# Kernel tuning notes

Measured on AMD Instinct MI355X. Metric: run time of the kernel, lower is better.

## Reference

```python
import jax, jax.numpy as jnp
import numpy as np

K = 3      # kernel size
PAD = 1    # padding
EPS = 1e-5 # BatchNorm eps


def conv3x3(x, w, b):
    out = jax.lax.conv_general_dilated(
        x, w, window_strides=(1, 1), padding=((PAD, PAD), (PAD, PAD)),
        dimension_numbers=('NCHW', 'OIHW', 'NCHW'))
    return out + b[None, :, None, None]


def bilinear_gather(x, py, px):
    # x: [B,C,H,W]; py,px: [B,K2,H,W] fractional sample coords (zero pad OOB)
    B, C, H, W = x.shape
    y0 = jnp.floor(py)
    x0 = jnp.floor(px)
    wy1 = py - y0
    wx1 = px - x0
    xf = x.reshape(B, C, H * W)

    def corner(yc, xc, wgt):
        valid = (yc >= 0) & (yc <= H - 1) & (xc >= 0) & (xc <= W - 1)
        yi = jnp.clip(yc, 0, H - 1).astype(jnp.int32)
        xi = jnp.clip(xc, 0, W - 1).astype(jnp.int32)
        idx = yi * W + xi                      # [B,K2,H,W]
        g = jax.vmap(lambda img, ix: jnp.take(img, ix, axis=1))(xf, idx.reshape(B, -1))
        g = g.reshape(B, C, idx.shape[1], H, W)  # [B,C,K2,H,W]
        return g * (wgt * valid)[:, None]

    return (corner(y0,     x0,     (1 - wy1) * (1 - wx1))
            + corner(y0,     x0 + 1, (1 - wy1) * wx1)
            + corner(y0 + 1, x0,     wy1 * (1 - wx1))
            + corner(y0 + 1, x0 + 1, wy1 * wx1))


def deform_conv_bn_relu(x, offset_w, offset_b, mod_w, mod_b, weight, bias, gamma, beta):
    B, Ci, H, W = x.shape
    Co = weight.shape[0]
    K2 = K * K
    # offset / modulator branches (dense 3x3 convs)
    off = conv3x3(x, offset_w, offset_b)                  # [B,2*K2,H,W]
    mask = 2.0 * jax.nn.sigmoid(conv3x3(x, mod_w, mod_b))  # [B,K2,H,W]
    off = off.reshape(B, K2, 2, H, W)
    dy, dx = off[:, :, 0], off[:, :, 1]
    # base sampling grid per kernel tap
    ii, jj = jnp.meshgrid(jnp.arange(K), jnp.arange(K), indexing='ij')
    ky = ii.reshape(-1).astype(x.dtype)                    # [K2]
    kx = jj.reshape(-1).astype(x.dtype)
    hh = jnp.arange(H, dtype=x.dtype)
    ww = jnp.arange(W, dtype=x.dtype)
    py = hh[None, None, :, None] - PAD + ky[None, :, None, None] + dy  # [B,K2,H,W]
    px = ww[None, None, None, :] - PAD + kx[None, :, None, None] + dx
    sampled = bilinear_gather(x, py, px)                   # [B,Ci,K2,H,W]
    sampled = sampled * mask[:, None]                      # modulated (DCNv2)
    out = jnp.einsum('bckhw,ock->bohw', sampled, weight.reshape(Co, Ci, K2))
    out = out + bias[None, :, None, None]
    # BatchNorm (batch statistics) + ReLU
    mu = out.mean(axis=(0, 2, 3), keepdims=True)
    var = out.var(axis=(0, 2, 3), keepdims=True)
    y = (out - mu) * jax.lax.rsqrt(var + EPS) * gamma[None, :, None, None] + beta[None, :, None, None]
    return jax.nn.relu(y)


def setup_inputs() -> dict:
    key = jax.random.key(0)
    ks = jax.random.split(key, 4)
    B, Ci, Co, H, W = 8, 256, 256, 64, 64
    x = jax.random.normal(ks[0], (B, Ci, H, W), jnp.float32)
    offset_w = jax.random.normal(ks[1], (2 * K * K, Ci, K, K), jnp.float32) * 0.01
    offset_b = jnp.zeros((2 * K * K,), jnp.float32)
    mod_w = jax.random.normal(ks[2], (K * K, Ci, K, K), jnp.float32) * 0.01
    mod_b = jnp.zeros((K * K,), jnp.float32)
    weight = jax.random.normal(ks[3], (Co, Ci, K, K), jnp.float32) * (1.0 / np.sqrt(Ci * K * K))
    bias = jnp.zeros((Co,), jnp.float32)
    gamma = jnp.ones((Co,), jnp.float32)
    beta = jnp.zeros((Co,), jnp.float32)
    return {"x": x, "offset_w": offset_w, "offset_b": offset_b,
            "mod_w": mod_w, "mod_b": mod_b, "weight": weight, "bias": bias,
            "gamma": gamma, "beta": beta}


def reference(x, offset_w, offset_b, mod_w, mod_b, weight, bias, gamma, beta):
    return deform_conv_bn_relu(x, offset_w, offset_b, mod_w, mod_b, weight, bias, gamma, beta)
```

## Files before the change

kernel.cpp:

```cpp
#include <hip/hip_runtime.h>
#include <math.h>

#define CI 256
#define CO 256
#define HWN 4096

typedef short bf16x8 __attribute__((ext_vector_type(8)));
typedef float f32x4 __attribute__((ext_vector_type(4)));

__device__ inline unsigned pk2(float a, float b) {
  unsigned ua = __float_as_uint(a), ub = __float_as_uint(b);
  ua += 0x7fff + ((ua >> 16) & 1);
  ub += 0x7fff + ((ub >> 16) & 1);
  return (ua >> 16) | (ub & 0xffff0000u);
}

#define PIPE_BARRIER()                                    \
  do {                                                    \
    __builtin_amdgcn_sched_barrier(0);                    \
    asm volatile("s_waitcnt lgkmcnt(0)" ::: "memory");    \
    __builtin_amdgcn_s_barrier();                         \
    __builtin_amdgcn_sched_barrier(0);                    \
  } while (0)

__global__ __launch_bounds__(256) void k_xprep(const float4* __restrict__ xf,
                                               uint4* __restrict__ xh) {
  int i = blockIdx.x * 256 + threadIdx.x;
  float4 a = xf[2 * i], b = xf[2 * i + 1];
  xh[i] = make_uint4(pk2(a.x, a.y), pk2(a.z, a.w), pk2(b.x, b.y),
                     pk2(b.z, b.w));
}

__global__ __launch_bounds__(256) void k_wprep(const float* __restrict__ wgt,
                                               unsigned short* __restrict__ wT) {
  const int o = blockIdx.x, c = threadIdx.x;
  const float* wp = wgt + o * 2304 + c * 9;
  float v[9];
#pragma unroll
  for (int t = 0; t < 9; ++t) v[t] = wp[t];
#pragma unroll
  for (int t = 0; t < 9; ++t) {
    unsigned u = __float_as_uint(v[t]);
    u += 0x7fff + ((u >> 16) & 1);
    wT[(t << 16) + (o << 8) + c] = (unsigned short)(u >> 16);
  }
}

__global__ __launch_bounds__(256) void k_woprep(
    const float* __restrict__ ow, const float* __restrict__ mw,
    unsigned short* __restrict__ wTo) {
  const int o = blockIdx.x, c = threadIdx.x;
  float v[9];
  if (o < 18) {
    const float* wp = ow + o * 2304 + c * 9;
#pragma unroll
    for (int t = 0; t < 9; ++t) v[t] = wp[t];
  } else if (o < 27) {
    const float* wp = mw + (o - 18) * 2304 + c * 9;
#pragma unroll
    for (int t = 0; t < 9; ++t) v[t] = wp[t];
  } else {
#pragma unroll
    for (int t = 0; t < 9; ++t) v[t] = 0.f;
  }
#pragma unroll
  for (int t = 0; t < 9; ++t) {
    unsigned u = __float_as_uint(v[t]);
    u += 0x7fff + ((u >> 16) & 1);
    wTo[(t << 13) + (o << 8) + c] = (unsigned short)(u >> 16);
  }
}

__global__ __launch_bounds__(256, 4) void k_offmod_m(
    const unsigned short* __restrict__ xh, const unsigned short* __restrict__ wTo,
    const float* __restrict__ ob, const float* __restrict__ mb,
    float* __restrict__ dyb, float* __restrict__ dxb,
    float* __restrict__ mskb) {
  __shared__ __align__(16) unsigned s_cwo[576];
  __shared__ unsigned short s_cio[576];
  __shared__ __align__(16) char sA[8192];
  __shared__ __align__(16) char sB[4096];

  const int tid = threadIdx.x;
  const int bid = blockIdx.x;
  const int b = bid >> 6, h = bid & 63;
  const int lane = tid & 63;
  const int wv = tid >> 6;
  const int px = lane;

  for (int i = tid; i < 576; i += 256) {
    int k = i >> 6, pxi = i & 63;
    int ky = k / 3, kx = k - 3 * ky;
    int y0 = h - 1 + ky;
    int x0 = pxi - 1 + kx;
    bool vy = ((unsigned)y0 < 64u);
    bool vx = ((unsigned)x0 < 64u);
    float w00 = (vy && vx) ? 1.f : 0.f;
    int y0c = min(max(y0, 0), 63);
    int xp = min(max(x0, 0), 62);
    int s0 = min(max(x0, 0), 63) - xp;
    float a = s0 ? 0.f : w00;
    float bb = s0 ? w00 : 0.f;
    s_cwo[i] = pk2(a, bb);
    s_cio[i] = (unsigned short)(y0c * 64 + xp);
  }
  __syncthreads();

  f32x4 acc[2];
  acc[0] = (f32x4){0.f, 0.f, 0.f, 0.f};
  acc[1] = (f32x4){0.f, 0.f, 0.f, 0.f};

  const char* xbh = (const char*)(xh + (size_t)b * (CI * HWN));

  unsigned rxu[16];
  float cwA, cwB;
  {
    unsigned p = s_cwo[px];
    cwA = __uint_as_float(p << 16);
    cwB = __uint_as_float(p & 0xffff0000u);
    int ci = s_cio[px];
#pragma unroll
    for (int g2 = 0; g2 < 2; ++g2) {
      int g = wv + (g2 << 2);
#pragma unroll
      for (int j = 0; j < 8; ++j) {
        int c = (g << 3) + j;
        __builtin_memcpy(&rxu[(g2 << 3) + j], xbh + (((c << 12) + ci) << 1), 4);
      }
    }
  }

#pragma unroll 1
  for (int t = 0; t < 36; ++t) {
    const int cq = t / 9;
    const int tap = t - cq * 9;
#pragma unroll
    for (int g2 = 0; g2 < 2; ++g2) {
      unsigned pkv[4];
#pragma unroll
      for (int j2 = 0; j2 < 4; ++j2) {
        unsigned d0 = rxu[(g2 << 3) + (j2 << 1)];
        unsigned d1 = rxu[(g2 << 3) + (j2 << 1) + 1];
        float v0 = cwA * __uint_as_float(d0 << 16);
        v0 = fmaf(cwB, __uint_as_float(d0 & 0xffff0000u), v0);
        float v1 = cwA * __uint_as_float(d1 << 16);
        v1 = fmaf(cwB, __uint_as_float(d1 & 0xffff0000u), v1);
        pkv[j2] = pk2(v0, v1);
      }
      int g = wv + (g2 << 2);
      *(uint4*)(sA + (px << 7) + ((g ^ (px & 7)) << 4)) =
          make_uint4(pkv[0], pkv[1], pkv[2], pkv[3]);
    }
    {
      int o = tid >> 3, seg = tid & 7;
      uint4 v = *(const uint4*)(wTo + (tap << 13) + (o << 8) + (cq << 6) +
                                (seg << 3));
      *(uint4*)(sB + (o << 7) + ((seg ^ (o & 7)) << 4)) = v;
    }
    {
      const int tn = t < 35 ? t + 1 : 35;
      const int cqn = tn / 9;
      const int tapn = tn - cqn * 9;
      unsigned p = s_cwo[(tapn << 6) + px];
      float cwAn = __uint_as_float(p << 16);
      float cwBn = __uint_as_float(p & 0xffff0000u);
      int ci = s_cio[(tapn << 6) + px];
#pragma unroll
      for (int g2 = 0; g2 < 2; ++g2) {
        int g = wv + (g2 << 2);
#pragma unroll
        for (int j = 0; j < 8; ++j) {
          int c = (cqn << 6) + (g << 3) + j;
          __builtin_memcpy(&rxu[(g2 << 3) + j], xbh + (((c << 12) + ci) << 1),
                           4);
        }
      }
      cwA = cwAn;
      cwB = cwBn;
    }
    PIPE_BARRIER();
#pragma unroll
    for (int ks = 0; ks < 2; ++ks) {
      int arow = (wv << 4) + (lane & 15);
      int aslt = ((ks << 2) + (lane >> 4)) ^ (arow & 7);
      bf16x8 af = *(bf16x8*)(sA + (arow << 7) + (aslt << 4));
#pragma unroll
      for (int nf = 0; nf < 2; ++nf) {
        int brow = (nf << 4) + (lane & 15);
        int bslt = ((ks << 2) + (lane >> 4)) ^ (brow & 7);
        bf16x8 bfr = *(bf16x8*)(sB + (brow << 7) + (bslt << 4));
        acc[nf] = __builtin_amdgcn_mfma_f32_16x16x32_bf16(af, bfr, acc[nf], 0,
                                                          0, 0);
      }
    }
    PIPE_BARRIER();
  }

#pragma unroll
  for (int nf = 0; nf < 2; ++nf) {
    int o = (nf << 4) + (lane & 15);
    int px0 = (wv << 4) + ((lane >> 4) << 2);
    if (o < 18) {
      float bo = ob[o];
      float4 v = make_float4(acc[nf][0] + bo, acc[nf][1] + bo, acc[nf][2] + bo,
                             acc[nf][3] + bo);
      float* dst = (o & 1) ? dxb : dyb;
      int k = o >> 1;
      *(float4*)(dst + ((b * 9 + k) << 12) + (h << 6) + px0) = v;
    } else if (o < 27) {
      float bm = mb[o - 18];
      float4 v;
      v.x = 2.f / (1.f + expf(-(acc[nf][0] + bm)));
      v.y = 2.f / (1.f + expf(-(acc[nf][1] + bm)));
      v.z = 2.f / (1.f + expf(-(acc[nf][2] + bm)));
      v.w = 2.f / (1.f + expf(-(acc[nf][3] + bm)));
      *(float4*)(mskb + ((b * 9 + (o - 18)) << 12) + (h << 6) + px0) = v;
    }
  }
}

__global__ __launch_bounds__(512, 4) void k_offmod_fb(
    const float* __restrict__ x, const float* __restrict__ ow,
    const float* __restrict__ ob, const float* __restrict__ mw,
    const float* __restrict__ mb, float* __restrict__ dyb,
    float* __restrict__ dxb, float* __restrict__ mskb) {
  __shared__ float ps[13824];
  const int tid = threadIdx.x;
  const int bid = blockIdx.x;
  const int b = bid & 7;
  const int h = bid >> 3;
  const int cg = __builtin_amdgcn_readfirstlane(tid >> 6);
  const int px = tid & 63;
  float acc[27];
#pragma unroll
  for (int i = 0; i < 27; ++i) acc[i] = 0.f;

  const float* xb = x + b * (CI * HWN);
  const int h0c = max(h - 1, 0), h2c = min(h + 1, 63);
  const bool v0 = h > 0, v2 = h < 63;
  const bool e0 = (px == 0), e63 = (px == 63);
  const float* xw = xb + (cg << 5) * HWN;

#pragma unroll 1
  for (int i = 0; i < 32; ++i) {
    const float* xc = xw + i * HWN;
    float c0 = xc[h0c * 64 + px];
    float c1 = xc[h * 64 + px];
    float c2 = xc[h2c * 64 + px];
    c0 = v0 ? c0 : 0.f;
    c2 = v2 ? c2 : 0.f;
    float l0 = __shfl_up(c0, 1), l1 = __shfl_up(c1, 1), l2 = __shfl_up(c2, 1);
    float r0 = __shfl_down(c0, 1), r1 = __shfl_down(c1, 1),
          r2 = __shfl_down(c2, 1);
    l0 = e0 ? 0.f : l0;
    l1 = e0 ? 0.f : l1;
    l2 = e0 ? 0.f : l2;
    r0 = e63 ? 0.f : r0;
    r1 = e63 ? 0.f : r1;
    r2 = e63 ? 0.f : r2;
    float xv[9] = {l0, c0, r0, l1, c1, r1, l2, c2, r2};
    const int c = (cg << 5) + i;
    const float* owp = ow + c * 9;
    const float* mwp = mw + c * 9;
#pragma unroll
    for (int ch = 0; ch < 18; ++ch)
#pragma unroll
      for (int k = 0; k < 9; ++k)
        acc[ch] = fmaf(owp[ch * 2304 + k], xv[k], acc[ch]);
#pragma unroll
    for (int ch = 0; ch < 9; ++ch)
#pragma unroll
      for (int k = 0; k < 9; ++k)
        acc[18 + ch] = fmaf(mwp[ch * 2304 + k], xv[k], acc[18 + ch]);
  }

#pragma unroll
  for (int ch = 0; ch < 27; ++ch) ps[(px * 27 + ch) * 8 + cg] = acc[ch];
  __syncthreads();
  for (int i = tid; i < 1728; i += 512) {
    int p2 = i / 27;
    int ch = i - p2 * 27;
    float s = 0.f;
#pragma unroll
    for (int g = 0; g < 8; ++g) s += ps[i * 8 + g];
    if (ch < 18) {
      s += ob[ch];
      int k = ch >> 1;
      int o9 = ((b * 9 + k) << 12) + (h << 6) + p2;
      if ((ch & 1) == 0) dyb[o9] = s;
      else dxb[o9] = s;
    } else {
      int k = ch - 18;
      s += mb[k];
      mskb[((b * 9 + k) << 12) + (h << 6) + p2] = 2.f / (1.f + expf(-s));
    }
  }
}

__global__ __launch_bounds__(512, 4) void k_main_h(
    const unsigned short* __restrict__ xh, const unsigned short* __restrict__ wT,
    const float* __restrict__ dyb, const float* __restrict__ dxb,
    const float* __restrict__ mskb, float* __restrict__ out,
    float* __restrict__ psum, float* __restrict__ psq) {
  __shared__ __align__(16) char smem[47872];
  uint2* s_cw = (uint2*)smem;
  ushort2* s_ci = (ushort2*)(smem + 4608);
  char* sA = smem + 6912;
  char* sB = smem + 15104;
  float* tr = (float*)(smem + 6912);

  const int tid = threadIdx.x;
  const int mblk = blockIdx.x;
  const int b = mblk >> 6, h = mblk & 63;
  const int lane = tid & 63;
  const int wv = tid >> 6;

  for (int i = tid; i < 576; i += 512) {
    int k = i >> 6, pxi = i & 63;
    int o9 = ((b * 9 + k) << 12) + (h << 6) + pxi;
    float m = mskb[o9];
    float py = (float)(h - 1 + k / 3) + dyb[o9];
    float pxf = (float)(pxi - 1 + k % 3) + dxb[o9];
    float y0f = floorf(py), x0f = floorf(pxf);
    float wy = py - y0f, wx = pxf - x0f;
    int y0 = (int)y0f, x0 = (int)x0f;
    int y1 = y0 + 1, x1 = x0 + 1;
    float w00 = (1.f - wy) * (1.f - wx) * m;
    float w01 = (1.f - wy) * wx * m;
    float w10 = wy * (1.f - wx) * m;
    float w11 = wy * wx * m;
    bool vy0 = ((unsigned)y0 < 64u), vy1 = ((unsigned)y1 < 64u);
    bool vx0 = ((unsigned)x0 < 64u), vx1 = ((unsigned)x1 < 64u);
    if (!(vy0 && vx0)) w00 = 0.f;
    if (!(vy0 && vx1)) w01 = 0.f;
    if (!(vy1 && vx0)) w10 = 0.f;
    if (!(vy1 && vx1)) w11 = 0.f;
    int y0c = min(max(y0, 0), 63), y1c = min(max(y1, 0), 63);
    int x0c = min(max(x0, 0), 63), x1c = min(max(x1, 0), 63);
    int xp = min(max(x0, 0), 62);
    int s0 = x0c - xp, s1 = x1c - xp;
    float a0 = (s0 ? 0.f : w00) + (s1 ? 0.f : w01);
    float b0 = (s0 ? w00 : 0.f) + (s1 ? w01 : 0.f);
    float a1 = (s0 ? 0.f : w10) + (s1 ? 0.f : w11);
    float b1 = (s0 ? w10 : 0.f) + (s1 ? w11 : 0.f);
    s_cw[i] = make_uint2(pk2(a0, b0), pk2(a1, b1));
    s_ci[i] = make_ushort2((unsigned short)(y0c * 64 + xp),
                           (unsigned short)(y1c * 64 + xp));
  }
  __syncthreads();

  f32x4 acc[4][2];
#pragma unroll
  for (int mf = 0; mf < 4; ++mf)
#pragma unroll
    for (int nf = 0; nf < 2; ++nf) acc[mf][nf] = (f32x4){0.f, 0.f, 0.f, 0.f};

  const char* xbh = (const char*)(xh + (size_t)b * (CI * HWN));
  const int aslot = (lane << 7) + ((wv ^ (lane & 7)) << 4);

  unsigned rxu[16];
  float4 cwC;
  {
    uint2 p = s_cw[lane];
    cwC.x = __uint_as_float(p.x << 16);
    cwC.y = __uint_as_float(p.x & 0xffff0000u);
    cwC.z = __uint_as_float(p.y << 16);
    cwC.w = __uint_as_float(p.y & 0xffff0000u);
    ushort2 ci0 = s_ci[lane];
    const char* xcn = xbh + (((wv << 3) * HWN) << 1);
#pragma unroll
    for (int s = 0; s < 8; ++s) {
      const char* xc = xcn + ((s * HWN) << 1);
      __builtin_memcpy(&rxu[2 * s + 0], xc + ((int)ci0.x << 1), 4);
      __builtin_memcpy(&rxu[2 * s + 1], xc + ((int)ci0.y << 1), 4);
    }
  }

#pragma unroll 1
  for (int t = 0; t < 36; ++t) {
    const int cq = t / 9;
    const int tap = t - cq * 9;
    {
      unsigned pkv[4];
#pragma unroll
      for (int j2 = 0; j2 < 4; ++j2) {
        float vv[2];
#pragma unroll
        for (int u = 0; u < 2; ++u) {
          unsigned d0 = rxu[4 * j2 + 2 * u], d1 = rxu[4 * j2 + 2 * u + 1];
          float v = cwC.x * __uint_as_float(d0 << 16);
          v = fmaf(cwC.y, __uint_as_float(d0 & 0xffff0000u), v);
          v = fmaf(cwC.z, __uint_as_float(d1 << 16), v);
          vv[u] = fmaf(cwC.w, __uint_as_float(d1 & 0xffff0000u), v);
        }
        pkv[j2] = pk2(vv[0], vv[1]);
      }
      *(uint4*)(sA + aslot) = make_uint4(pkv[0], pkv[1], pkv[2], pkv[3]);
    }
    {
      const unsigned short* wp = wT + (tap << 16) + (cq << 6);
#pragma unroll
      for (int r = 0; r < 4; ++r) {
        int idx = (r << 9) + tid;
        int o = idx >> 3, seg = idx & 7;
        uint4 v = *(const uint4*)(wp + (o << 8) + (seg << 3));
        int slot = seg ^ (o & 7);
        *(uint4*)(sB + (o << 7) + (slot << 4)) = v;
      }
    }
    {
      const int tn = t < 35 ? t + 1 : 35;
      const int cqn = tn / 9;
      const int tapn = tn - cqn * 9;
      uint2 p = s_cw[(tapn << 6) + lane];
      float4 cwN;
      cwN.x = __uint_as_float(p.x << 16);
      cwN.y = __uint_as_float(p.x & 0xffff0000u);
      cwN.z = __uint_as_float(p.y << 16);
      cwN.w = __uint_as_float(p.y & 0xffff0000u);
      ushort2 ciN = s_ci[(tapn << 6) + lane];
      const char* xcn = xbh + ((((cqn << 3) + wv) << 3) * HWN << 1);
#pragma unroll
      for (int s = 0; s < 8; ++s) {
        const char* xc = xcn + ((s * HWN) << 1);
        __builtin_memcpy(&rxu[2 * s + 0], xc + ((int)ciN.x << 1), 4);
        __builtin_memcpy(&rxu[2 * s + 1], xc + ((int)ciN.y << 1), 4);
      }
      cwC = cwN;
    }
    PIPE_BARRIER();
#pragma unroll
    for (int ks = 0; ks < 2; ++ks) {
      bf16x8 af[4], bfr[2];
#pragma unroll
      for (int mf = 0; mf < 4; ++mf) {
        int row = (mf << 4) + (lane & 15);
        int slot = ((ks << 2) + (lane >> 4)) ^ (row & 7);
        af[mf] = *(bf16x8*)(sA + (row << 7) + (slot << 4));
      }
#pragma unroll
      for (int nf = 0; nf < 2; ++nf) {
        int row = (wv << 5) + (nf << 4) + (lane & 15);
        int slot = ((ks << 2) + (lane >> 4)) ^ (row & 7);
        bfr[nf] = *(bf16x8*)(sB + (row << 7) + (slot << 4));
      }
#pragma unroll
      for (int mf = 0; mf < 4; ++mf)
#pragma unroll
        for (int nf = 0; nf < 2; ++nf)
          acc[mf][nf] = __builtin_amdgcn_mfma_f32_16x16x32_bf16(
              af[mf], bfr[nf], acc[mf][nf], 0, 0, 0);
    }
    PIPE_BARRIER();
  }

#pragma unroll
  for (int nf = 0; nf < 2; ++nf) {
    float s = 0.f, q = 0.f;
#pragma unroll
    for (int mf = 0; mf < 4; ++mf)
#pragma unroll
      for (int r = 0; r < 4; ++r) {
        float v = acc[mf][nf][r];
        s += v;
        q = fmaf(v, v, q);
      }
    s += __shfl_down(s, 32);
    q += __shfl_down(q, 32);
    s += __shfl_down(s, 16);
    q += __shfl_down(q, 16);
    if (lane < 16) {
      int o = (wv << 5) + (nf << 4) + lane;
      psum[(o << 9) + mblk] = s;
      psq[(o << 9) + mblk] = q;
    }
  }

  __syncthreads();
  for (int p = 0; p < 2; ++p) {
    if ((wv >> 2) == p) {
#pragma unroll
      for (int mf = 0; mf < 4; ++mf)
#pragma unroll
        for (int nf = 0; nf < 2; ++nf) {
          int ro = ((wv & 3) << 5) + (nf << 4) + (lane & 15);
#pragma unroll
          for (int r = 0; r < 4; ++r)
            tr[ro * 65 + (mf << 4) + ((lane >> 4) << 2) + r] = acc[mf][nf][r];
        }
    }
    __syncthreads();
#pragma unroll
    for (int it = 0; it < 4; ++it) {
      int idx = tid + (it << 9);
      int ro = idx >> 4, qd = idx & 15;
      float4 v = make_float4(tr[ro * 65 + qd * 4], tr[ro * 65 + qd * 4 + 1],
                             tr[ro * 65 + qd * 4 + 2], tr[ro * 65 + qd * 4 + 3]);
      *(float4*)(out + (((b << 8) + (p << 7) + ro) << 12) + (h << 6) +
                 (qd << 2)) = v;
    }
    __syncthreads();
  }
}

__global__ __launch_bounds__(512, 4) void k_main_f32(
    const float* __restrict__ x, const unsigned short* __restrict__ wT,
    const float* __restrict__ dyb, const float* __restrict__ dxb,
    const float* __restrict__ mskb, float* __restrict__ out,
    float* __restrict__ psum, float* __restrict__ psq) {
  __shared__ __align__(16) char smem[50176];
  uint2* s_cw = (uint2*)smem;
  ushort4* s_ci = (ushort4*)(smem + 4608);
  char* sA = smem + 9216;
  char* sB = smem + 17408;
  float* tr = (float*)(smem + 9216);

  const int tid = threadIdx.x;
  const int mblk = blockIdx.x;
  const int b = mblk >> 6, h = mblk & 63;
  const int lane = tid & 63;
  const int wv = tid >> 6;

  for (int i = tid; i < 576; i += 512) {
    int k = i >> 6, pxi = i & 63;
    int o9 = ((b * 9 + k) << 12) + (h << 6) + pxi;
    float m = mskb[o9];
    float py = (float)(h - 1 + k / 3) + dyb[o9];
    float pxf = (float)(pxi - 1 + k % 3) + dxb[o9];
    float y0f = floorf(py), x0f = floorf(pxf);
    float wy = py - y0f, wx = pxf - x0f;
    int y0 = (int)y0f, x0 = (int)x0f;
    int y1 = y0 + 1, x1 = x0 + 1;
    float w00 = (1.f - wy) * (1.f - wx) * m;
    float w01 = (1.f - wy) * wx * m;
    float w10 = wy * (1.f - wx) * m;
    float w11 = wy * wx * m;
    bool vy0 = ((unsigned)y0 < 64u), vy1 = ((unsigned)y1 < 64u);
    bool vx0 = ((unsigned)x0 < 64u), vx1 = ((unsigned)x1 < 64u);
    if (!(vy0 && vx0)) w00 = 0.f;
    if (!(vy0 && vx1)) w01 = 0.f;
    if (!(vy1 && vx0)) w10 = 0.f;
    if (!(vy1 && vx1)) w11 = 0.f;
    int y0c = min(max(y0, 0), 63), y1c = min(max(y1, 0), 63);
    int x0c = min(max(x0, 0), 63), x1c = min(max(x1, 0), 63);
    s_cw[i] = make_uint2(pk2(w00, w01), pk2(w10, w11));
    s_ci[i] = make_ushort4((unsigned short)(y0c * 64 + x0c),
                           (unsigned short)(y0c * 64 + x1c),
                           (unsigned short)(y1c * 64 + x0c),
                           (unsigned short)(y1c * 64 + x1c));
  }
  __syncthreads();

  f32x4 acc[4][2];
#pragma unroll
// ... 170 lines not shown
    q += __shfl_down(q, off, 64);
  }
  if (t == 0) {
    const float inv_n = 1.f / 32768.f;
    float mean = s * inv_n;
    float var = fmaf(-mean, mean, q * inv_n);
    float sc = gamma[o] * rsqrtf(var + 1e-5f);
    scale[o] = sc;
    shift[o] = fmaf(-mean, sc, beta[o]);
  }
}

__global__ __launch_bounds__(256) void k_bnrelu(
    float* __restrict__ out, const float* __restrict__ scale,
    const float* __restrict__ shift) {
  int idx = blockIdx.x * 256 + threadIdx.x;
  int o = (idx >> 10) & 255;
  float sc = scale[o], sh = shift[o];
  float4 v = ((float4*)out)[idx];
  v.x = fmaxf(fmaf(v.x, sc, sh), 0.f);
  v.y = fmaxf(fmaf(v.y, sc, sh), 0.f);
  v.z = fmaxf(fmaf(v.z, sc, sh), 0.f);
  v.w = fmaxf(fmaf(v.w, sc, sh), 0.f);
  ((float4*)out)[idx] = v;
}

extern "C" void kernel_launch(void* const* d_in, const int* in_sizes, int n_in,
                              void* d_out, int out_size, void* d_ws,
                              size_t ws_size, hipStream_t stream) {
  const float* x = (const float*)d_in[0];
  const float* ow = (const float*)d_in[1];
  const float* ob = (const float*)d_in[2];
  const float* mw = (const float*)d_in[3];
  const float* mb = (const float*)d_in[4];
  const float* wgt = (const float*)d_in[5];
  const float* gamma = (const float*)d_in[7];
  const float* beta = (const float*)d_in[8];
  float* out = (float*)d_out;

  float* ws = (float*)d_ws;
  float* dyb = ws;
  float* dxb = dyb + 294912;
  float* mskb = dxb + 294912;
  float* psum = mskb + 294912;
  float* psq = psum + 131072;
  float* scale = psq + 131072;
  float* shift = scale + 256;
  unsigned short* wT = (unsigned short*)(shift + 256);
  unsigned short* xhp = wT + 589824;
  unsigned short* wTo = xhp + 8388608;
  const size_t WS_NEED = (size_t)(294912 * 3 + 131072 * 2 + 512) * 4 +
                         589824 * 2 + 8388608 * 2 + 73728 * 2;

  k_wprep<<<256, 256, 0, stream>>>(wgt, wT);
  if (ws_size >= WS_NEED) {
    k_woprep<<<32, 256, 0, stream>>>(ow, mw, wTo);
    k_xprep<<<4096, 256, 0, stream>>>((const float4*)x, (uint4*)xhp);
    k_offmod_m<<<512, 256, 0, stream>>>(xhp, wTo, ob, mb, dyb, dxb, mskb);
    k_main_h<<<512, 512, 0, stream>>>(xhp, wT, dyb, dxb, mskb, out, psum, psq);
  } else {
    k_offmod_fb<<<512, 512, 0, stream>>>(x, ow, ob, mw, mb, dyb, dxb, mskb);
    k_main_f32<<<512, 512, 0, stream>>>(x, wT, dyb, dxb, mskb, out, psum, psq);
  }
  k_stats<<<256, 64, 0, stream>>>(psum, psq, gamma, beta, scale, shift);
  k_bnrelu<<<8192, 256, 0, stream>>>(out, scale, shift);
}
```

Baseline: 197.0 us.

## Double-buffer gather registers and issue weight loads early in main deform GEMM loop

Restructures the k_main_h loop into a macro that is unrolled twice, ping-ponging two register buffers so the next tap's gathers land in the other buffer without a copy. Weight tile global loads are now issued into registers at the start of each chunk and written to LDS after the bilinear blending, which hides their latency behind the ALU work. Block indexing also changes so consecutive blocks cover different batches at the same row, which alters cache locality. The cost is higher register pressure under launch_bounds(512,4) and possible spills.

```diff
diff --git a/kernel.cpp b/kernel.cpp
--- a/kernel.cpp
+++ b/kernel.cpp
@@ -297,6 +297,80 @@
   }
 }
 
+#define KCHUNK(T, RXP, RXI)                                                   \
+  {                                                                           \
+    const int cq_ = (T) / 9;                                                  \
+    const int tap_ = (T)-cq_ * 9;                                             \
+    uint4 rb_[4];                                                             \
+    {                                                                         \
+      const unsigned short* wp_ = wT + (tap_ << 16) + (cq_ << 6);             \
+      _Pragma("unroll") for (int r = 0; r < 4; ++r) {                         \
+        int idx_ = (r << 9) + tid;                                            \
+        int o_ = idx_ >> 3, seg_ = idx_ & 7;                                  \
+        rb_[r] = *(const uint4*)(wp_ + (o_ << 8) + (seg_ << 3));              \
+      }                                                                       \
+    }                                                                         \
+    {                                                                         \
+      const int tn_ = (T) < 35 ? (T) + 1 : 35;                                \
+      const int cqn_ = tn_ / 9;                                               \
+      const int tapn_ = tn_ - cqn_ * 9;                                       \
+      ushort2 ciN_ = s_ci[(tapn_ << 6) + lane];                               \
+      const char* xcn_ = xbh + ((((cqn_ << 3) + wv) << 3) * HWN << 1);        \
+      _Pragma("unroll") for (int s = 0; s < 8; ++s) {                         \
+        const char* xc_ = xcn_ + ((s * HWN) << 1);                            \
+        __builtin_memcpy(&RXI[2 * s + 0], xc_ + ((int)ciN_.x << 1), 4);       \
+        __builtin_memcpy(&RXI[2 * s + 1], xc_ + ((int)ciN_.y << 1), 4);       \
+      }                                                                       \
+    }                                                                         \
+    {                                                                         \
+      uint2 p_ = s_cw[(tap_ << 6) + lane];                                    \
+      float cwx_ = __uint_as_float(p_.x << 16);                               \
+      float cwy_ = __uint_as_float(p_.x & 0xffff0000u);                       \
+      float cwz_ = __uint_as_float(p_.y << 16);                               \
+      float cww_ = __uint_as_float(p_.y & 0xffff0000u);                       \
+      unsigned pkv_[4];                                                       \
+      _Pragma("unroll") for (int j2 = 0; j2 < 4; ++j2) {                      \
+        unsigned d0_ = RXP[4 * j2 + 0], d1_ = RXP[4 * j2 + 1];                \
+        float v_ = cwx_ * __uint_as_float(d0_ << 16);                         \
+        v_ = fmaf(cwy_, __uint_as_float(d0_ & 0xffff0000u), v_);              \
+        v_ = fmaf(cwz_, __uint_as_float(d1_ << 16), v_);                      \
+        float vv0_ = fmaf(cww_, __uint_as_float(d1_ & 0xffff0000u), v_);      \
+        unsigned d2_ = RXP[4 * j2 + 2], d3_ = RXP[4 * j2 + 3];                \
+        float w_ = cwx_ * __uint_as_float(d2_ << 16);                         \
+        w_ = fmaf(cwy_, __uint_as_float(d2_ & 0xffff0000u), w_);              \
+        w_ = fmaf(cwz_, __uint_as_float(d3_ << 16), w_);                      \
+        float vv1_ = fmaf(cww_, __uint_as_float(d3_ & 0xffff0000u), w_);      \
+        pkv_[j2] = pk2(vv0_, vv1_);                                           \
+      }                                                                       \
+      *(uint4*)(sA + aslot) = make_uint4(pkv_[0], pkv_[1], pkv_[2], pkv_[3]); \
+    }                                                                         \
+    _Pragma("unroll") for (int r = 0; r < 4; ++r) {                           \
+      int idx_ = (r << 9) + tid;                                              \
+      int o_ = idx_ >> 3, seg_ = idx_ & 7;                                    \
+      int slot_ = seg_ ^ (o_ & 7);                                            \
+      *(uint4*)(sB + (o_ << 7) + (slot_ << 4)) = rb_[r];                      \
+    }                                                                         \
+    PIPE_BARRIER();                                                           \
+    _Pragma("unroll") for (int ks = 0; ks < 2; ++ks) {                        \
+      bf16x8 af_[4], bfr_[2];                                                 \
+      _Pragma("unroll") for (int mf = 0; mf < 4; ++mf) {                      \
+        int row_ = (mf << 4) + (lane & 15);                                   \
+        int slot_ = ((ks << 2) + (lane >> 4)) ^ (row_ & 7);                   \
+        af_[mf] = *(bf16x8*)(sA + (row_ << 7) + (slot_ << 4));                \
+      }                                                                       \
+      _Pragma("unroll") for (int nf = 0; nf < 2; ++nf) {                      \
+        int row_ = (wv << 5) + (nf << 4) + (lane & 15);                       \
+        int slot_ = ((ks << 2) + (lane >> 4)) ^ (row_ & 7);                   \
+        bfr_[nf] = *(bf16x8*)(sB + (row_ << 7) + (slot_ << 4));               \
+      }                                                                       \
+      _Pragma("unroll") for (int mf = 0; mf < 4; ++mf)                        \
+          _Pragma("unroll") for (int nf = 0; nf < 2; ++nf)                    \
+              acc[mf][nf] = __builtin_amdgcn_mfma_f32_16x16x32_bf16(          \
+                  af_[mf], bfr_[nf], acc[mf][nf], 0, 0, 0);                   \
+    }                                                                         \
+    PIPE_BARRIER();                                                           \
+  }
+
 __global__ __launch_bounds__(512, 4) void k_main_h(
     const unsigned short* __restrict__ xh, const unsigned short* __restrict__ wT,
     const float* __restrict__ dyb, const float* __restrict__ dxb,
@@ -311,7 +385,7 @@
 
   const int tid = threadIdx.x;
   const int mblk = blockIdx.x;
-  const int b = mblk >> 6, h = mblk & 63;
+  const int b = mblk & 7, h = mblk >> 3;
   const int lane = tid & 63;
   const int wv = tid >> 6;
 
@@ -358,100 +432,22 @@
   const char* xbh = (const char*)(xh + (size_t)b * (CI * HWN));
   const int aslot = (lane << 7) + ((wv ^ (lane & 7)) << 4);
 
-  unsigned rxu[16];
-  float4 cwC;
+  unsigned rxA[16], rxB[16];
   {
-    uint2 p = s_cw[lane];
-    cwC.x = __uint_as_float(p.x << 16);
-    cwC.y = __uint_as_float(p.x & 0xffff0000u);
-    cwC.z = __uint_as_float(p.y << 16);
-    cwC.w = __uint_as_float(p.y & 0xffff0000u);
     ushort2 ci0 = s_ci[lane];
     const char* xcn = xbh + (((wv << 3) * HWN) << 1);
 #pragma unroll
     for (int s = 0; s < 8; ++s) {
       const char* xc = xcn + ((s * HWN) << 1);
-      __builtin_memcpy(&rxu[2 * s + 0], xc + ((int)ci0.x << 1), 4);
-      __builtin_memcpy(&rxu[2 * s + 1], xc + ((int)ci0.y << 1), 4);
+      __builtin_memcpy(&rxA[2 * s + 0], xc + ((int)ci0.x << 1), 4);
+      __builtin_memcpy(&rxA[2 * s + 1], xc + ((int)ci0.y << 1), 4);
     }
   }
 
 #pragma unroll 1
-  for (int t = 0; t < 36; ++t) {
-    const int cq = t / 9;
-    const int tap = t - cq * 9;
-    {
-      unsigned pkv[4];
-#pragma unroll
-      for (int j2 = 0; j2 < 4; ++j2) {
-        float vv[2];
-#pragma unroll
-        for (int u = 0; u < 2; ++u) {
-          unsigned d0 = rxu[4 * j2 + 2 * u], d1 = rxu[4 * j2 + 2 * u + 1];
-          float v = cwC.x * __uint_as_float(d0 << 16);
-          v = fmaf(cwC.y, __uint_as_float(d0 & 0xffff0000u), v);
-          v = fmaf(cwC.z, __uint_as_float(d1 << 16), v);
-          vv[u] = fmaf(cwC.w, __uint_as_float(d1 & 0xffff0000u), v);
-        }
-        pkv[j2] = pk2(vv[0], vv[1]);
-      }
-      *(uint4*)(sA + aslot) = make_uint4(pkv[0], pkv[1], pkv[2], pkv[3]);
-    }
-    {
-      const unsigned short* wp = wT + (tap << 16) + (cq << 6);
-#pragma unroll
-      for (int r = 0; r < 4; ++r) {
-        int idx = (r << 9) + tid;
-        int o = idx >> 3, seg = idx & 7;
-        uint4 v = *(const uint4*)(wp + (o << 8) + (seg << 3));
-        int slot = seg ^ (o & 7);
-        *(uint4*)(sB + (o << 7) + (slot << 4)) = v;
-      }
-    }
-    {
-      const int tn = t < 35 ? t + 1 : 35;
-      const int cqn = tn / 9;
-      const int tapn = tn - cqn * 9;
-      uint2 p = s_cw[(tapn << 6) + lane];
-      float4 cwN;
-      cwN.x = __uint_as_float(p.x << 16);
-      cwN.y = __uint_as_float(p.x & 0xffff0000u);
-      cwN.z = __uint_as_float(p.y << 16);
-      cwN.w = __uint_as_float(p.y & 0xffff0000u);
-      ushort2 ciN = s_ci[(tapn << 6) + lane];
-      const char* xcn = xbh + ((((cqn << 3) + wv) << 3) * HWN << 1);
-#pragma unroll
-      for (int s = 0; s < 8; ++s) {
-        const char* xc = xcn + ((s * HWN) << 1);
-        __builtin_memcpy(&rxu[2 * s + 0], xc + ((int)ciN.x << 1), 4);
-        __builtin_memcpy(&rxu[2 * s + 1], xc + ((int)ciN.y << 1), 4);
-      }
-      cwC = cwN;
-    }
-    PIPE_BARRIER();
-#pragma unroll
-    for (int ks = 0; ks < 2; ++ks) {
-      bf16x8 af[4], bfr[2];
-#pragma unroll
-      for (int mf = 0; mf < 4; ++mf) {
-        int row = (mf << 4) + (lane & 15);
-        int slot = ((ks << 2) + (lane >> 4)) ^ (row & 7);
-        af[mf] = *(bf16x8*)(sA + (row << 7) + (slot << 4));
-      }
-#pragma unroll
-      for (int nf = 0; nf < 2; ++nf) {
-        int row = (wv << 5) + (nf << 4) + (lane & 15);
-        int slot = ((ks << 2) + (lane >> 4)) ^ (row & 7);
-        bfr[nf] = *(bf16x8*)(sB + (row << 7) + (slot << 4));
-      }
-#pragma unroll
-      for (int mf = 0; mf < 4; ++mf)
-#pragma unroll
-        for (int nf = 0; nf < 2; ++nf)
-          acc[mf][nf] = __builtin_amdgcn_mfma_f32_16x16x32_bf16(
-              af[mf], bfr[nf], acc[mf][nf], 0, 0, 0);
-    }
-    PIPE_BARRIER();
+  for (int t2 = 0; t2 < 36; t2 += 2) {
+    KCHUNK(t2, rxA, rxB);
+    KCHUNK(t2 + 1, rxB, rxA);
   }
 
 #pragma unroll
```

New measurement: 203.2 us. +3.1%, slower.

## Fuse offset/modulator conv into main deform kernel and merge prep kernels

Applied to the files above, without the earlier changes.

The three prep kernels (x to bf16, main weights, offset/mod weights) are merged into a single launch. The offset/modulator MFMA conv now runs at the start of the main deformable-conv kernel. Its 512 threads are split into two groups that each reduce half the channels, and the partial sums are combined through shared memory. Offsets and mask stay in LDS instead of making a round trip through global memory, which removes two launches and the dy/dx/mask global traffic, in exchange for a longer prologue in each main-kernel block.

```diff
diff --git a/kernel.cpp b/kernel.cpp
--- a/kernel.cpp
+++ b/kernel.cpp
@@ -23,284 +23,58 @@
     __builtin_amdgcn_sched_barrier(0);                    \
   } while (0)
 
-__global__ __launch_bounds__(256) void k_xprep(const float4* __restrict__ xf,
-                                               uint4* __restrict__ xh) {
-  int i = blockIdx.x * 256 + threadIdx.x;
-  float4 a = xf[2 * i], b = xf[2 * i + 1];
-  xh[i] = make_uint4(pk2(a.x, a.y), pk2(a.z, a.w), pk2(b.x, b.y),
-                     pk2(b.z, b.w));
+__global__ __launch_bounds__(256) void k_prep(
+    const float* __restrict__ x, const float* __restrict__ wgt,
+    const float* __restrict__ ow, const float* __restrict__ mw,
+    unsigned short* __restrict__ wT, unsigned short* __restrict__ wTo,
+    unsigned short* __restrict__ xhp) {
+  const int bid = blockIdx.x, tid = threadIdx.x;
+  if (bid < 4096) {
+    int i = bid * 256 + tid;
+    const float4* xf = (const float4*)x;
+    float4 a = xf[2 * i], b = xf[2 * i + 1];
+    ((uint4*)xhp)[i] = make_uint4(pk2(a.x, a.y), pk2(a.z, a.w), pk2(b.x, b.y),
+                                  pk2(b.z, b.w));
+  } else if (bid < 4352) {
+    int o = bid - 4096, c = tid;
+    const float* wp = wgt + o * 2304 + c * 9;
+    float v[9];
+#pragma unroll
+    for (int t = 0; t < 9; ++t) v[t] = wp[t];
+#pragma unroll
+    for (int t = 0; t < 9; ++t) {
+      unsigned u = __float_as_uint(v[t]);
+      u += 0x7fff + ((u >> 16) & 1);
+      wT[(t << 16) + (o << 8) + c] = (unsigned short)(u >> 16);
+    }
+  } else {
+    int o = bid - 4352, c = tid;
+    float v[9];
+    if (o < 18) {
+      const float* wp = ow + o * 2304 + c * 9;
+#pragma unroll
+      for (int t = 0; t < 9; ++t) v[t] = wp[t];
+    } else if (o < 27) {
+      const float* wp = mw + (o - 18) * 2304 + c * 9;
+#pragma unroll
+      for (int t = 0; t < 9; ++t) v[t] = wp[t];
+    } else {
+#pragma unroll
+      for (int t = 0; t < 9; ++t) v[t] = 0.f;
+    }
+#pragma unroll
+    for (int t = 0; t < 9; ++t) {
+      unsigned u = __float_as_uint(v[t]);
+      u += 0x7fff + ((u >> 16) & 1);
+      wTo[(t << 13) + (o << 8) + c] = (unsigned short)(u >> 16);
+    }
+  }
 }
 
-__global__ __launch_bounds__(256) void k_wprep(const float* __restrict__ wgt,
-                                               unsigned short* __restrict__ wT) {
-  const int o = blockIdx.x, c = threadIdx.x;
-  const float* wp = wgt + o * 2304 + c * 9;
-  float v[9];
-#pragma unroll
-  for (int t = 0; t < 9; ++t) v[t] = wp[t];
-#pragma unroll
-  for (int t = 0; t < 9; ++t) {
-    unsigned u = __float_as_uint(v[t]);
-    u += 0x7fff + ((u >> 16) & 1);
-    wT[(t << 16) + (o << 8) + c] = (unsigned short)(u >> 16);
-  }
-}
-
-__global__ __launch_bounds__(256) void k_woprep(
-    const float* __restrict__ ow, const float* __restrict__ mw,
-    unsigned short* __restrict__ wTo) {
-  const int o = blockIdx.x, c = threadIdx.x;
-  float v[9];
-  if (o < 18) {
-    const float* wp = ow + o * 2304 + c * 9;
-#pragma unroll
-    for (int t = 0; t < 9; ++t) v[t] = wp[t];
-  } else if (o < 27) {
-    const float* wp = mw + (o - 18) * 2304 + c * 9;
-#pragma unroll
-    for (int t = 0; t < 9; ++t) v[t] = wp[t];
-  } else {
-#pragma unroll
-    for (int t = 0; t < 9; ++t) v[t] = 0.f;
-  }
-#pragma unroll
-  for (int t = 0; t < 9; ++t) {
-    unsigned u = __float_as_uint(v[t]);
-    u += 0x7fff + ((u >> 16) & 1);
-    wTo[(t << 13) + (o << 8) + c] = (unsigned short)(u >> 16);
-  }
-}
-
-__global__ __launch_bounds__(256, 4) void k_offmod_m(
-    const unsigned short* __restrict__ xh, const unsigned short* __restrict__ wTo,
-    const float* __restrict__ ob, const float* __restrict__ mb,
-    float* __restrict__ dyb, float* __restrict__ dxb,
-    float* __restrict__ mskb) {
-  __shared__ __align__(16) unsigned s_cwo[576];
-  __shared__ unsigned short s_cio[576];
-  __shared__ __align__(16) char sA[8192];
-  __shared__ __align__(16) char sB[4096];
-
-  const int tid = threadIdx.x;
-  const int bid = blockIdx.x;
-  const int b = bid >> 6, h = bid & 63;
-  const int lane = tid & 63;
-  const int wv = tid >> 6;
-  const int px = lane;
-
-  for (int i = tid; i < 576; i += 256) {
-    int k = i >> 6, pxi = i & 63;
-    int ky = k / 3, kx = k - 3 * ky;
-    int y0 = h - 1 + ky;
-    int x0 = pxi - 1 + kx;
-    bool vy = ((unsigned)y0 < 64u);
-    bool vx = ((unsigned)x0 < 64u);
-    float w00 = (vy && vx) ? 1.f : 0.f;
-    int y0c = min(max(y0, 0), 63);
-    int xp = min(max(x0, 0), 62);
-    int s0 = min(max(x0, 0), 63) - xp;
-    float a = s0 ? 0.f : w00;
-    float bb = s0 ? w00 : 0.f;
-    s_cwo[i] = pk2(a, bb);
-    s_cio[i] = (unsigned short)(y0c * 64 + xp);
-  }
-  __syncthreads();
-
-  f32x4 acc[2];
-  acc[0] = (f32x4){0.f, 0.f, 0.f, 0.f};
-  acc[1] = (f32x4){0.f, 0.f, 0.f, 0.f};
-
-  const char* xbh = (const char*)(xh + (size_t)b * (CI * HWN));
-
-  unsigned rxu[16];
-  float cwA, cwB;
-  {
-    unsigned p = s_cwo[px];
-    cwA = __uint_as_float(p << 16);
-    cwB = __uint_as_float(p & 0xffff0000u);
-    int ci = s_cio[px];
-#pragma unroll
-    for (int g2 = 0; g2 < 2; ++g2) {
-      int g = wv + (g2 << 2);
-#pragma unroll
-      for (int j = 0; j < 8; ++j) {
-        int c = (g << 3) + j;
-        __builtin_memcpy(&rxu[(g2 << 3) + j], xbh + (((c << 12) + ci) << 1), 4);
-      }
-    }
-  }
-
-#pragma unroll 1
-  for (int t = 0; t < 36; ++t) {
-    const int cq = t / 9;
-    const int tap = t - cq * 9;
-#pragma unroll
-    for (int g2 = 0; g2 < 2; ++g2) {
-      unsigned pkv[4];
-#pragma unroll
-      for (int j2 = 0; j2 < 4; ++j2) {
-        unsigned d0 = rxu[(g2 << 3) + (j2 << 1)];
-        unsigned d1 = rxu[(g2 << 3) + (j2 << 1) + 1];
-        float v0 = cwA * __uint_as_float(d0 << 16);
-        v0 = fmaf(cwB, __uint_as_float(d0 & 0xffff0000u), v0);
-        float v1 = cwA * __uint_as_float(d1 << 16);
-        v1 = fmaf(cwB, __uint_as_float(d1 & 0xffff0000u), v1);
-        pkv[j2] = pk2(v0, v1);
-      }
-      int g = wv + (g2 << 2);
-      *(uint4*)(sA + (px << 7) + ((g ^ (px & 7)) << 4)) =
-          make_uint4(pkv[0], pkv[1], pkv[2], pkv[3]);
-    }
-    {
-      int o = tid >> 3, seg = tid & 7;
-      uint4 v = *(const uint4*)(wTo + (tap << 13) + (o << 8) + (cq << 6) +
-                                (seg << 3));
-      *(uint4*)(sB + (o << 7) + ((seg ^ (o & 7)) << 4)) = v;
-    }
-    {
-      const int tn = t < 35 ? t + 1 : 35;
-      const int cqn = tn / 9;
-      const int tapn = tn - cqn * 9;
-      unsigned p = s_cwo[(tapn << 6) + px];
-      float cwAn = __uint_as_float(p << 16);
-      float cwBn = __uint_as_float(p & 0xffff0000u);
-      int ci = s_cio[(tapn << 6) + px];
-#pragma unroll
-      for (int g2 = 0; g2 < 2; ++g2) {
-        int g = wv + (g2 << 2);
-#pragma unroll
-        for (int j = 0; j < 8; ++j) {
-          int c = (cqn << 6) + (g << 3) + j;
-          __builtin_memcpy(&rxu[(g2 << 3) + j], xbh + (((c << 12) + ci) << 1),
-                           4);
-        }
-      }
-      cwA = cwAn;
-      cwB = cwBn;
-    }
-    PIPE_BARRIER();
-#pragma unroll
-    for (int ks = 0; ks < 2; ++ks) {
-      int arow = (wv << 4) + (lane & 15);
-      int aslt = ((ks << 2) + (lane >> 4)) ^ (arow & 7);
-      bf16x8 af = *(bf16x8*)(sA + (arow << 7) + (aslt << 4));
-#pragma unroll
-      for (int nf = 0; nf < 2; ++nf) {
-        int brow = (nf << 4) + (lane & 15);
-        int bslt = ((ks << 2) + (lane >> 4)) ^ (brow & 7);
-        bf16x8 bfr = *(bf16x8*)(sB + (brow << 7) + (bslt << 4));
-        acc[nf] = __builtin_amdgcn_mfma_f32_16x16x32_bf16(af, bfr, acc[nf], 0,
-                                                          0, 0);
-      }
-    }
-    PIPE_BARRIER();
-  }
-
-#pragma unroll
-  for (int nf = 0; nf < 2; ++nf) {
-    int o = (nf << 4) + (lane & 15);
-    int px0 = (wv << 4) + ((lane >> 4) << 2);
-    if (o < 18) {
-      float bo = ob[o];
-      float4 v = make_float4(acc[nf][0] + bo, acc[nf][1] + bo, acc[nf][2] + bo,
-                             acc[nf][3] + bo);
-      float* dst = (o & 1) ? dxb : dyb;
-      int k = o >> 1;
-      *(float4*)(dst + ((b * 9 + k) << 12) + (h << 6) + px0) = v;
-    } else if (o < 27) {
-      float bm = mb[o - 18];
-      float4 v;
-      v.x = 2.f / (1.f + expf(-(acc[nf][0] + bm)));
-      v.y = 2.f / (1.f + expf(-(acc[nf][1] + bm)));
-      v.z = 2.f / (1.f + expf(-(acc[nf][2] + bm)));
-      v.w = 2.f / (1.f + expf(-(acc[nf][3] + bm)));
-      *(float4*)(mskb + ((b * 9 + (o - 18)) << 12) + (h << 6) + px0) = v;
-    }
-  }
-}
-
-__global__ __launch_bounds__(512, 4) void k_offmod_fb(
-    const float* __restrict__ x, const float* __restrict__ ow,
-    const float* __restrict__ ob, const float* __restrict__ mw,
-    const float* __restrict__ mb, float* __restrict__ dyb,
-    float* __restrict__ dxb, float* __restrict__ mskb) {
-  __shared__ float ps[13824];
-  const int tid = threadIdx.x;
-  const int bid = blockIdx.x;
-  const int b = bid & 7;
-  const int h = bid >> 3;
-  const int cg = __builtin_amdgcn_readfirstlane(tid >> 6);
-  const int px = tid & 63;
-  float acc[27];
-#pragma unroll
-  for (int i = 0; i < 27; ++i) acc[i] = 0.f;
-
-  const float* xb = x + b * (CI * HWN);
-  const int h0c = max(h - 1, 0), h2c = min(h + 1, 63);
-  const bool v0 = h > 0, v2 = h < 63;
-  const bool e0 = (px == 0), e63 = (px == 63);
-  const float* xw = xb + (cg << 5) * HWN;
-
-#pragma unroll 1
-  for (int i = 0; i < 32; ++i) {
-    const float* xc = xw + i * HWN;
-    float c0 = xc[h0c * 64 + px];
-    float c1 = xc[h * 64 + px];
-    float c2 = xc[h2c * 64 + px];
-    c0 = v0 ? c0 : 0.f;
-    c2 = v2 ? c2 : 0.f;
-    float l0 = __shfl_up(c0, 1), l1 = __shfl_up(c1, 1), l2 = __shfl_up(c2, 1);
-    float r0 = __shfl_down(c0, 1), r1 = __shfl_down(c1, 1),
-          r2 = __shfl_down(c2, 1);
-    l0 = e0 ? 0.f : l0;
-    l1 = e0 ? 0.f : l1;
-    l2 = e0 ? 0.f : l2;
-    r0 = e63 ? 0.f : r0;
-    r1 = e63 ? 0.f : r1;
-    r2 = e63 ? 0.f : r2;
-    float xv[9] = {l0, c0, r0, l1, c1, r1, l2, c2, r2};
-    const int c = (cg << 5) + i;
-    const float* owp = ow + c * 9;
-    const float* mwp = mw + c * 9;
-#pragma unroll
-    for (int ch = 0; ch < 18; ++ch)
-#pragma unroll
-      for (int k = 0; k < 9; ++k)
-        acc[ch] = fmaf(owp[ch * 2304 + k], xv[k], acc[ch]);
-#pragma unroll
-    for (int ch = 0; ch < 9; ++ch)
-#pragma unroll
-      for (int k = 0; k < 9; ++k)
-        acc[18 + ch] = fmaf(mwp[ch * 2304 + k], xv[k], acc[18 + ch]);
-  }
-
-#pragma unroll
-  for (int ch = 0; ch < 27; ++ch) ps[(px * 27 + ch) * 8 + cg] = acc[ch];
-  __syncthreads();
-  for (int i = tid; i < 1728; i += 512) {
-    int p2 = i / 27;
-    int ch = i - p2 * 27;
-    float s = 0.f;
-#pragma unroll
-    for (int g = 0; g < 8; ++g) s += ps[i * 8 + g];
-    if (ch < 18) {
-      s += ob[ch];
-      int k = ch >> 1;
-      int o9 = ((b * 9 + k) << 12) + (h << 6) + p2;
-      if ((ch & 1) == 0) dyb[o9] = s;
-      else dxb[o9] = s;
-    } else {
-      int k = ch - 18;
-      s += mb[k];
-      mskb[((b * 9 + k) << 12) + (h << 6) + p2] = 2.f / (1.f + expf(-s));
-    }
-  }
-}
-
-__global__ __launch_bounds__(512, 4) void k_main_h(
+__global__ __launch_bounds__(512, 4) void k_fused2(
     const unsigned short* __restrict__ xh, const unsigned short* __restrict__ wT,
-    const float* __restrict__ dyb, const float* __restrict__ dxb,
-    const float* __restrict__ mskb, float* __restrict__ out,
+    const unsigned short* __restrict__ wTo, const float* __restrict__ ob,
+    const float* __restrict__ mb, float* __restrict__ out,
     float* __restrict__ psum, float* __restrict__ psq) {
   __shared__ __align__(16) char smem[47872];
   uint2* s_cw = (uint2*)smem;
@@ -308,19 +82,167 @@
   char* sA = smem + 6912;
   char* sB = smem + 15104;
   float* tr = (float*)(smem + 6912);
+  char* sA0 = smem + 6912;
+  char* sA1 = smem + 15104;
+  char* sB0 = smem + 23296;
+  char* sB1 = smem + 27392;
+  float* s_red = (float*)(smem + 6912);
+  float* s_off = (float*)(smem + 31488);
 
   const int tid = threadIdx.x;
   const int mblk = blockIdx.x;
   const int b = mblk >> 6, h = mblk & 63;
   const int lane = tid & 63;
   const int wv = tid >> 6;
+  const char* xbh = (const char*)(xh + (size_t)b * (CI * HWN));
+
+  {
+    const int grp = wv >> 2;
+    const int lw = wv & 3;
+    const int gtid = tid & 255;
+    const int px = lane;
+    char* sAg = grp ? sA1 : sA0;
+    char* sBg = grp ? sB1 : sB0;
+    f32x4 pacc[2];
+    pacc[0] = (f32x4){0.f, 0.f, 0.f, 0.f};
+    pacc[1] = (f32x4){0.f, 0.f, 0.f, 0.f};
+
+    unsigned rxu[16];
+    float cwA, cwB;
+    {
+      int y0 = h - 1, x0 = px - 1;
+      float w = (((unsigned)y0 < 64u) && ((unsigned)x0 < 64u)) ? 1.f : 0.f;
+      int y0c = min(max(y0, 0), 63);
+      int xp = min(max(x0, 0), 62);
+      int s0 = min(max(x0, 0), 63) - xp;
+      cwA = s0 ? 0.f : w;
+      cwB = s0 ? w : 0.f;
+      int ci = y0c * 64 + xp;
+#pragma unroll
+      for (int g2 = 0; g2 < 2; ++g2) {
+        int g = lw + (g2 << 2);
+#pragma unroll
+        for (int j = 0; j < 8; ++j) {
+          int c = ((grp << 1) << 6) + (g << 3) + j;
+          __builtin_memcpy(&rxu[(g2 << 3) + j], xbh + (((c << 12) + ci) << 1),
+                           4);
+        }
+      }
+    }
+
+#pragma unroll 1
+    for (int t = 0; t < 18; ++t) {
+      const int cqi = t / 9;
+      const int tap = t - cqi * 9;
+      const int cq = (grp << 1) + cqi;
+#pragma unroll
+      for (int g2 = 0; g2 < 2; ++g2) {
+        unsigned pkv[4];
+#pragma unroll
+        for (int j2 = 0; j2 < 4; ++j2) {
+          unsigned d0 = rxu[(g2 << 3) + (j2 << 1)];
+          unsigned d1 = rxu[(g2 << 3) + (j2 << 1) + 1];
+          float v0 = cwA * __uint_as_float(d0 << 16);
+          v0 = fmaf(cwB, __uint_as_float(d0 & 0xffff0000u), v0);
+          float v1 = cwA * __uint_as_float(d1 << 16);
+          v1 = fmaf(cwB, __uint_as_float(d1 & 0xffff0000u), v1);
+          pkv[j2] = pk2(v0, v1);
+        }
+        int g = lw + (g2 << 2);
+        *(uint4*)(sAg + (px << 7) + ((g ^ (px & 7)) << 4)) =
+            make_uint4(pkv[0], pkv[1], pkv[2], pkv[3]);
+      }
+      {
+        int o = gtid >> 3, seg = gtid & 7;
+        uint4 v = *(const uint4*)(wTo + (tap << 13) + (o << 8) + (cq << 6) +
+                                  (seg << 3));
+        *(uint4*)(sBg + (o << 7) + ((seg ^ (o & 7)) << 4)) = v;
+      }
+      {
+        const int tn = t < 17 ? t + 1 : 17;
+        const int cqni = tn / 9;
+        const int tapn = tn - cqni * 9;
+        const int cqn = (grp << 1) + cqni;
+        int ky = tapn / 3, kx = tapn - 3 * ky;
+        int y0 = h - 1 + ky, x0 = px - 1 + kx;
+        float w = (((unsigned)y0 < 64u) && ((unsigned)x0 < 64u)) ? 1.f : 0.f;
+        int y0c = min(max(y0, 0), 63);
+        int xp = min(max(x0, 0), 62);
+        int s0 = min(max(x0, 0), 63) - xp;
+        float cwAn = s0 ? 0.f : w;
+        float cwBn = s0 ? w : 0.f;
+        int ci = y0c * 64 + xp;
+#pragma unroll
+        for (int g2 = 0; g2 < 2; ++g2) {
+          int g = lw + (g2 << 2);
+#pragma unroll
+          for (int j = 0; j < 8; ++j) {
+            int c = (cqn << 6) + (g << 3) + j;
+            __builtin_memcpy(&rxu[(g2 << 3) + j],
+                             xbh + (((c << 12) + ci) << 1), 4);
+          }
+        }
+        cwA = cwAn;
+        cwB = cwBn;
+      }
+      PIPE_BARRIER();
+#pragma unroll
+      for (int ks = 0; ks < 2; ++ks) {
+        int arow = (lw << 4) + (lane & 15);
+        int aslt = ((ks << 2) + (lane >> 4)) ^ (arow & 7);
+        bf16x8 af = *(bf16x8*)(sAg + (arow << 7) + (aslt << 4));
+#pragma unroll
+        for (int nf = 0; nf < 2; ++nf) {
+          int brow = (nf << 4) + (lane & 15);
+          int bslt = ((ks << 2) + (lane >> 4)) ^ (brow & 7);
+          bf16x8 bfr = *(bf16x8*)(sBg + (brow << 7) + (bslt << 4));
+          pacc[nf] = __builtin_amdgcn_mfma_f32_16x16x32_bf16(af, bfr, pacc[nf],
+                                                             0, 0, 0);
+        }
+      }
+      PIPE_BARRIER();
+    }
+    if (grp == 1) {
+#pragma unroll
+      for (int nf = 0; nf < 2; ++nf)
+#pragma unroll
+        for (int r = 0; r < 4; ++r) s_red[gtid * 8 + nf * 4 + r] = pacc[nf][r];
+    }
+    __syncthreads();
+    if (grp == 0) {
+#pragma unroll
+      for (int nf = 0; nf < 2; ++nf) {
+#pragma unroll
+        for (int r = 0; r < 4; ++r)
+          pacc[nf][r] += s_red[gtid * 8 + nf * 4 + r];
+        int o = (nf << 4) + (lane & 15);
+        int px0 = (lw << 4) + ((lane >> 4) << 2);
+        if (o < 18) {
+          float bo = ob[o];
+          *(float4*)(s_off + o * 64 + px0) =
+              make_float4(pacc[nf][0] + bo, pacc[nf][1] + bo, pacc[nf][2] + bo,
+                          pacc[nf][3] + bo);
+        } else if (o < 27) {
+          float bm = mb[o - 18];
+          float4 v;
+          v.x = 2.f / (1.f + expf(-(pacc[nf][0] + bm)));
+          v.y = 2.f / (1.f + expf(-(pacc[nf][1] + bm)));
+          v.z = 2.f / (1.f + expf(-(pacc[nf][2] + bm)));
+          v.w = 2.f / (1.f + expf(-(pacc[nf][3] + bm)));
+          *(float4*)(s_off + o * 64 + px0) = v;
+        }
+      }
+    }
+    __syncthreads();
+  }
 
   for (int i = tid; i < 576; i += 512) {
     int k = i >> 6, pxi = i & 63;
-    int o9 = ((b * 9 + k) << 12) + (h << 6) + pxi;
-    float m = mskb[o9];
-    float py = (float)(h - 1 + k / 3) + dyb[o9];
-    float pxf = (float)(pxi - 1 + k % 3) + dxb[o9];
+    float dy = s_off[(2 * k) * 64 + pxi];
+    float dx = s_off[(2 * k + 1) * 64 + pxi];
+    float m = s_off[(18 + k) * 64 + pxi];
+    float py = (float)(h - 1 + k / 3) + dy;
+    float pxf = (float)(pxi - 1 + k % 3) + dx;
     float y0f = floorf(py), x0f = floorf(pxf);
     float wy = py - y0f, wx = pxf - x0f;
     int y0 = (int)y0f, x0 = (int)x0f;
@@ -355,7 +277,6 @@
 #pragma unroll
     for (int nf = 0; nf < 2; ++nf) acc[mf][nf] = (f32x4){0.f, 0.f, 0.f, 0.f};
 
-  const char* xbh = (const char*)(xh + (size_t)b * (CI * HWN));
   const int aslot = (lane << 7) + ((wv ^ (lane & 7)) << 4);
 
   unsigned rxu[16];
@@ -500,6 +421,99 @@
                  (qd << 2)) = v;
     }
     __syncthreads();
+  }
+}
+
+__global__ __launch_bounds__(256) void k_wprep(const float* __restrict__ wgt,
+                                               unsigned short* __restrict__ wT) {
+  const int o = blockIdx.x, c = threadIdx.x;
+  const float* wp = wgt + o * 2304 + c * 9;
+  float v[9];
+#pragma unroll
+  for (int t = 0; t < 9; ++t) v[t] = wp[t];
+#pragma unroll
+  for (int t = 0; t < 9; ++t) {
+    unsigned u = __float_as_uint(v[t]);
+    u += 0x7fff + ((u >> 16) & 1);
+    wT[(t << 16) + (o << 8) + c] = (unsigned short)(u >> 16);
+  }
+}
+
+__global__ __launch_bounds__(512, 4) void k_offmod_fb(
+    const float* __restrict__ x, const float* __restrict__ ow,
+    const float* __restrict__ ob, const float* __restrict__ mw,
+    const float* __restrict__ mb, float* __restrict__ dyb,
+    float* __restrict__ dxb, float* __restrict__ mskb) {
+  __shared__ float ps[13824];
+  const int tid = threadIdx.x;
+  const int bid = blockIdx.x;
+  const int b = bid & 7;
+  const int h = bid >> 3;
+  const int cg = __builtin_amdgcn_readfirstlane(tid >> 6);
+  const int px = tid & 63;
+  float acc[27];
+#pragma unroll
+  for (int i = 0; i < 27; ++i) acc[i] = 0.f;
+
+  const float* xb = x + b * (CI * HWN);
+  const int h0c = max(h - 1, 0), h2c = min(h + 1, 63);
+  const bool v0 = h > 0, v2 = h < 63;
+  const bool e0 = (px == 0), e63 = (px == 63);
+  const float* xw = xb + (cg << 5) * HWN;
+
+#pragma unroll 1
+  for (int i = 0; i < 32; ++i) {
+    const float* xc = xw + i * HWN;
+    float c0 = xc[h0c * 64 + px];
+    float c1 = xc[h * 64 + px];
+    float c2 = xc[h2c * 64 + px];
+    c0 = v0 ? c0 : 0.f;
+    c2 = v2 ? c2 : 0.f;
+    float l0 = __shfl_up(c0, 1), l1 = __shfl_up(c1, 1), l2 = __shfl_up(c2, 1);
+    float r0 = __shfl_down(c0, 1), r1 = __shfl_down(c1, 1),
+          r2 = __shfl_down(c2, 1);
+    l0 = e0 ? 0.f : l0;
+    l1 = e0 ? 0.f : l1;
+    l2 = e0 ? 0.f : l2;
+    r0 = e63 ? 0.f : r0;
+    r1 = e63 ? 0.f : r1;
+    r2 = e63 ? 0.f : r2;
+    float xv[9] = {l0, c0, r0, l1, c1, r1, l2, c2, r2};
+    const int c = (cg << 5) + i;
+    const float* owp = ow + c * 9;
+    const float* mwp = mw + c * 9;
+#pragma unroll
+    for (int ch = 0; ch < 18; ++ch)
+#pragma unroll
+      for (int k = 0; k < 9; ++k)
+        acc[ch] = fmaf(owp[ch * 2304 + k], xv[k], acc[ch]);
+#pragma unroll
+    for (int ch = 0; ch < 9; ++ch)
+#pragma unroll
+      for (int k = 0; k < 9; ++k)
+        acc[18 + ch] = fmaf(mwp[ch * 2304 + k], xv[k], acc[18 + ch]);
+  }
+
+#pragma unroll
+  for (int ch = 0; ch < 27; ++ch) ps[(px * 27 + ch) * 8 + cg] = acc[ch];
+  __syncthreads();
+  for (int i = tid; i < 1728; i += 512) {
+    int p2 = i / 27;
+    int ch = i - p2 * 27;
+    float s = 0.f;
+#pragma unroll
+    for (int g = 0; g < 8; ++g) s += ps[i * 8 + g];
+    if (ch < 18) {
+      s += ob[ch];
+      int k = ch >> 1;
+      int o9 = ((b * 9 + k) << 12) + (h << 6) + p2;
+      if ((ch & 1) == 0) dyb[o9] = s;
+      else dxb[o9] = s;
+    } else {
+      int k = ch - 18;
+      s += mb[k];
+      mskb[((b * 9 + k) << 12) + (h << 6) + p2] = 2.f / (1.f + expf(-s));
+    }
   }
 }
 
@@ -776,13 +790,11 @@
   const size_t WS_NEED = (size_t)(294912 * 3 + 131072 * 2 + 512) * 4 +
                          589824 * 2 + 8388608 * 2 + 73728 * 2;
 
-  k_wprep<<<256, 256, 0, stream>>>(wgt, wT);
   if (ws_size >= WS_NEED) {
-    k_woprep<<<32, 256, 0, stream>>>(ow, mw, wTo);
-    k_xprep<<<4096, 256, 0, stream>>>((const float4*)x, (uint4*)xhp);
-    k_offmod_m<<<512, 256, 0, stream>>>(xhp, wTo, ob, mb, dyb, dxb, mskb);
-    k_main_h<<<512, 512, 0, stream>>>(xhp, wT, dyb, dxb, mskb, out, psum, psq);
+    k_prep<<<4384, 256, 0, stream>>>(x, wgt, ow, mw, wT, wTo, xhp);
+    k_fused2<<<512, 512, 0, stream>>>(xhp, wT, wTo, ob, mb, out, psum, psq);
   } else {
+    k_wprep<<<256, 256, 0, stream>>>(wgt, wT);
     k_offmod_fb<<<512, 512, 0, stream>>>(x, ow, ob, mw, mb, dyb, dxb, mskb);
     k_main_f32<<<512, 512, 0, stream>>>(x, wT, dyb, dxb, mskb, out, psum, psq);
   }
```

Result: faster. 182.6 us, median of 3 (-7.3%).
